# Performance work log

Measured on AMD Instinct MI355X. Metric: run time of the kernel, lower is better.

The kernel has to match this reference:

```python
import jax, jax.numpy as jnp
import numpy as np

N_SRC0, N_DST0 = 200000, 40000
N_SRC1, N_DST1 = 40000, 8000
E0, E1 = 1000000, 80000
D_IN, D_HID, D_OUT = 256, 512, 256


def setup_inputs() -> dict:
    key = jax.random.key(0)
    ks = jax.random.split(key, 10)
    return {
        "feat": jax.random.normal(ks[0], (N_SRC0, D_IN), dtype=jnp.float32),
        "Wself0": jax.random.normal(ks[1], (D_IN, D_HID), dtype=jnp.float32) * 0.05,
        "Wneigh0": jax.random.normal(ks[2], (D_IN, D_HID), dtype=jnp.float32) * 0.05,
        "b0": jnp.zeros((D_HID,), dtype=jnp.float32),
        "Wself1": jax.random.normal(ks[3], (D_HID, D_OUT), dtype=jnp.float32) * 0.05,
        "Wneigh1": jax.random.normal(ks[4], (D_HID, D_OUT), dtype=jnp.float32) * 0.05,
        "b1": jnp.zeros((D_OUT,), dtype=jnp.float32),
        "edge_src0": jax.random.randint(ks[5], (E0,), 0, N_SRC0, dtype=jnp.int32),
        "edge_dst0": jax.random.randint(ks[6], (E0,), 0, N_DST0, dtype=jnp.int32),
        "edge_src1": jax.random.randint(ks[7], (E1,), 0, N_SRC1, dtype=jnp.int32),
        "edge_dst1": jax.random.randint(ks[8], (E1,), 0, N_DST1, dtype=jnp.int32),
    }


def _mean_agg(h_src, src, dst, n_dst):
    # gather src features along edges, segment-mean over dst nodes
    msg_sum = jax.ops.segment_sum(h_src[src], dst, num_segments=n_dst)  # [n_dst, d]
    deg = jax.ops.segment_sum(jnp.ones(dst.shape, h_src.dtype), dst, num_segments=n_dst)
    return msg_sum / jnp.maximum(deg, 1.0)[:, None]


def _sage_layer(h, src, dst, n_dst, W_self, W_neigh, b):
    # DGL SAGEConv(mean): fc_self(h_dst) + fc_neigh(mean_neighbors) + bias
    h_dst = h[:n_dst]
    h_neigh = _mean_agg(h, src, dst, n_dst)
    return h_dst @ W_self + h_neigh @ W_neigh + b


def reference(feat, Wself0, Wneigh0, b0, Wself1, Wneigh1, b1,
              edge_src0, edge_dst0, edge_src1, edge_dst1):
    h = _sage_layer(feat, edge_src0, edge_dst0, N_DST0, Wself0, Wneigh0, b0)
    h = jax.nn.relu(h)  # ReLU between layers, not after last
    h = _sage_layer(h, edge_src1, edge_dst1, N_DST1, Wself1, Wneigh1, b1)
    return h
```

## Files before the change

### kernel.cpp

```cpp
#include <hip/hip_runtime.h>

#define DEV __device__ __forceinline__

typedef float f32x4 __attribute__((ext_vector_type(4)));
typedef short s16x4 __attribute__((ext_vector_type(4)));
typedef short s16x8 __attribute__((ext_vector_type(8)));

DEV float bf2f(short s) {
  unsigned u = ((unsigned)(unsigned short)s) << 16;
  return __builtin_bit_cast(float, u);
}
DEV short f2bf(float f) {
  unsigned u = __builtin_bit_cast(unsigned, f);
  u += 0x7FFFu + ((u >> 16) & 1u);
  return (short)(u >> 16);
}

DEV void gld_lds16(const void* g, void* l) {
  __builtin_amdgcn_global_load_lds(
      (const __attribute__((address_space(1))) void*)g,
      (__attribute__((address_space(3))) void*)l, 16, 0, 0);
}

__global__ void f32_to_bf16_k(const float* __restrict__ in, short* __restrict__ out, long n) {
  long i = ((long)blockIdx.x * blockDim.x + threadIdx.x) * 8;
  long stride = (long)gridDim.x * blockDim.x * 8;
  for (; i < n; i += stride) {
    f32x4 v0 = *(const f32x4*)(in + i);
    f32x4 v1 = *(const f32x4*)(in + i + 4);
    s16x8 o;
    o[0] = f2bf(v0[0]); o[1] = f2bf(v0[1]); o[2] = f2bf(v0[2]); o[3] = f2bf(v0[3]);
    o[4] = f2bf(v1[0]); o[5] = f2bf(v1[1]); o[6] = f2bf(v1[2]); o[7] = f2bf(v1[3]);
    *(s16x8*)(out + i) = o;
  }
}

__global__ void build_wt2_k(const float* __restrict__ Ws0, const float* __restrict__ Wn0,
                            short* __restrict__ W0T,
                            const float* __restrict__ Ws1, const float* __restrict__ Wn1,
                            short* __restrict__ W1T, int* __restrict__ cntz) {
  const int b = blockIdx.x, tid = threadIdx.x;
  if (b < 1024) {
    int idx = b * 256 + tid;
    if (idx < 512 * 512) {
      int n = idx >> 9, k = idx & 511;
      float v = (k < 256) ? Ws0[(size_t)k * 512 + n] : Wn0[(size_t)(k - 256) * 512 + n];
      W0T[idx] = f2bf(v);
    }
  } else if (b < 2048) {
    int idx = (b - 1024) * 256 + tid;
    if (idx < 256 * 1024) {
      int n = idx >> 10, k = idx & 1023;
      float v = (k < 512) ? Ws1[(size_t)k * 256 + n] : Wn1[(size_t)(k - 512) * 256 + n];
      W1T[idx] = f2bf(v);
    }
  } else {
    for (int idx = (b - 2048) * 256 + tid; idx < 48000; idx += 188 * 256) cntz[idx] = 0;
  }
}

__global__ void fillp2_k(const int* __restrict__ es0, const int* __restrict__ ed0, int E0,
                         int* __restrict__ cnt0, int* __restrict__ bk0,
                         const int* __restrict__ es1, const int* __restrict__ ed1, int E1,
                         int* __restrict__ cnt1, int* __restrict__ bk1) {
  const int b = blockIdx.x, tid = threadIdx.x;
  if (b < 936) {
    for (int e = b * 256 + tid; e < E0; e += 936 * 256) {
      int d = ed0[e];
      int p = atomicAdd(&cnt0[d], 1);
      if (p < 64) bk0[(d << 6) + p] = es0[e];
    }
  } else {
    for (int e = (b - 936) * 256 + tid; e < E1; e += 88 * 256) {
      int d = ed1[e];
      int p = atomicAdd(&cnt1[d], 1);
      if (p < 48) bk1[d * 48 + p] = es1[e];
    }
  }
}

__global__ void agg_f32_256(const float* __restrict__ X, const int* __restrict__ cntA,
                            const int* __restrict__ bucket, short* __restrict__ out,
                            int n_dst) {
  int gw = (blockIdx.x * blockDim.x + threadIdx.x) >> 6;
  if (gw >= n_dst) return;
  int lane = threadIdx.x & 63;
  int start = gw << 6, cnt = cntA[gw];
  float a[4] = {0, 0, 0, 0}, b[4] = {0, 0, 0, 0};
  int i = 0;
  for (; i + 2 <= cnt; i += 2) {
    int s0 = bucket[start + i], s1 = bucket[start + i + 1];
    f32x4 v0 = *(const f32x4*)(X + (size_t)s0 * 256 + lane * 4);
    f32x4 v1 = *(const f32x4*)(X + (size_t)s1 * 256 + lane * 4);
#pragma unroll
    for (int j = 0; j < 4; ++j) { a[j] += v0[j]; b[j] += v1[j]; }
  }
  if (i < cnt) {
    int s0 = bucket[start + i];
    f32x4 v0 = *(const f32x4*)(X + (size_t)s0 * 256 + lane * 4);
#pragma unroll
    for (int j = 0; j < 4; ++j) a[j] += v0[j];
  }
  float inv = 1.0f / (float)(cnt > 0 ? cnt : 1);
  s16x4 o;
#pragma unroll
  for (int j = 0; j < 4; ++j) o[j] = f2bf((a[j] + b[j]) * inv);
  *(s16x4*)(out + (size_t)gw * 256 + lane * 4) = o;
}

__global__ void agg_bf16_256(const short* __restrict__ X, const int* __restrict__ cntA,
                             const int* __restrict__ bucket, short* __restrict__ out,
                             int n_dst) {
  int gw = (blockIdx.x * blockDim.x + threadIdx.x) >> 6;
  if (gw >= n_dst) return;
  int lane = threadIdx.x & 63;
  int half = lane >> 5;
  int cl = lane & 31;
  int start = gw << 6, cnt = cntA[gw];
  float a[8] = {0, 0, 0, 0, 0, 0, 0, 0}, b[8] = {0, 0, 0, 0, 0, 0, 0, 0};
  int i = 0;
  for (; i + 8 <= cnt; i += 8) {
    int s0 = bucket[start + i + half];
    int s1 = bucket[start + i + 2 + half];
    int s2 = bucket[start + i + 4 + half];
    int s3 = bucket[start + i + 6 + half];
    s16x8 v0 = *(const s16x8*)(X + (size_t)s0 * 256 + cl * 8);
    s16x8 v1 = *(const s16x8*)(X + (size_t)s1 * 256 + cl * 8);
    s16x8 v2 = *(const s16x8*)(X + (size_t)s2 * 256 + cl * 8);
    s16x8 v3 = *(const s16x8*)(X + (size_t)s3 * 256 + cl * 8);
#pragma unroll
    for (int j = 0; j < 8; ++j) {
      a[j] += bf2f(v0[j]); b[j] += bf2f(v1[j]);
      a[j] += bf2f(v2[j]); b[j] += bf2f(v3[j]);
    }
  }
  for (; i + 4 <= cnt; i += 4) {
    int s0 = bucket[start + i + half];
    int s1 = bucket[start + i + 2 + half];
    s16x8 v0 = *(const s16x8*)(X + (size_t)s0 * 256 + cl * 8);
    s16x8 v1 = *(const s16x8*)(X + (size_t)s1 * 256 + cl * 8);
#pragma unroll
    for (int j = 0; j < 8; ++j) { a[j] += bf2f(v0[j]); b[j] += bf2f(v1[j]); }
  }
  for (; i < cnt; i += 2) {
    int idx = i + half;
    if (idx < cnt) {
      int s0 = bucket[start + idx];
      s16x8 v0 = *(const s16x8*)(X + (size_t)s0 * 256 + cl * 8);
#pragma unroll
      for (int j = 0; j < 8; ++j) a[j] += bf2f(v0[j]);
    }
  }
  float inv = 1.0f / (float)(cnt > 0 ? cnt : 1);
  float r[8];
#pragma unroll
  for (int j = 0; j < 8; ++j) {
    float s = a[j] + b[j];
    r[j] = s + __shfl(s, lane ^ 32);
  }
  if (half == 0) {
    s16x8 o;
#pragma unroll
    for (int j = 0; j < 8; ++j) o[j] = f2bf(r[j] * inv);
    *(s16x8*)(out + (size_t)gw * 256 + cl * 8) = o;
  }
}

__global__ void agg_bf16_512(const short* __restrict__ X, const int* __restrict__ cntA,
                             const int* __restrict__ bucket, short* __restrict__ out,
                             int n_dst) {
  int gw = (blockIdx.x * blockDim.x + threadIdx.x) >> 6;
  if (gw >= n_dst) return;
  int lane = threadIdx.x & 63;
  int start = gw * 48, cnt = cntA[gw];
  float a[8] = {0, 0, 0, 0, 0, 0, 0, 0}, b[8] = {0, 0, 0, 0, 0, 0, 0, 0};
  float c[8] = {0, 0, 0, 0, 0, 0, 0, 0}, d[8] = {0, 0, 0, 0, 0, 0, 0, 0};
  int i = 0;
  for (; i + 4 <= cnt; i += 4) {
    int s0 = bucket[start + i], s1 = bucket[start + i + 1];
    int s2 = bucket[start + i + 2], s3 = bucket[start + i + 3];
    s16x8 v0 = *(const s16x8*)(X + (size_t)s0 * 512 + lane * 8);
    s16x8 v1 = *(const s16x8*)(X + (size_t)s1 * 512 + lane * 8);
    s16x8 v2 = *(const s16x8*)(X + (size_t)s2 * 512 + lane * 8);
    s16x8 v3 = *(const s16x8*)(X + (size_t)s3 * 512 + lane * 8);
#pragma unroll
    for (int j = 0; j < 8; ++j) {
      a[j] += bf2f(v0[j]); b[j] += bf2f(v1[j]);
      c[j] += bf2f(v2[j]); d[j] += bf2f(v3[j]);
    }
  }
  for (; i < cnt; ++i) {
    int s0 = bucket[start + i];
    s16x8 v0 = *(const s16x8*)(X + (size_t)s0 * 512 + lane * 8);
#pragma unroll
    for (int j = 0; j < 8; ++j) a[j] += bf2f(v0[j]);
  }
  float inv = 1.0f / (float)(cnt > 0 ? cnt : 1);
  s16x8 o;
#pragma unroll
  for (int j = 0; j < 8; ++j) o[j] = f2bf(((a[j] + b[j]) + (c[j] + d[j])) * inv);
  *(s16x8*)(out + (size_t)gw * 512 + lane * 8) = o;
}

template <int BM, int BN, bool RELU_BF16>
__global__ __launch_bounds__(256, 2) void gemm_k(
    const short* __restrict__ Aleft, const short* __restrict__ Aright,
    const short* __restrict__ Bt, const float* __restrict__ bias,
    void* __restrict__ Cout, int M, int N, int K, int KH) {
  constexpr int MFR = BM / 32;
  constexpr int NFR = BN / 32;
  constexpr int PA = BM / 32;
  constexpr int PB = BN / 32;
  __shared__ short As[BM * 64];
  __shared__ short Bs[BN * 64];
  const int tid = threadIdx.x;
  const int w = tid >> 6, lane = tid & 63;
  const int m0 = blockIdx.y * BM, n0 = blockIdx.x * BN;
  const int wr = w >> 1, wc = w & 1;
  const int lr = lane & 15, lk = (lane >> 4) << 3;

  f32x4 acc[MFR][NFR] = {};

  const int nkt = K >> 6;
  const int ktH = KH >> 6;
  const size_t ldA = (size_t)KH * 2;
  const size_t ldB = (size_t)K * 2;

  for (int kt = 0; kt < nkt; ++kt) {
    const char* Abase = (const char*)((kt < ktH) ? Aleft : Aright);
    const int ktl = (kt < ktH) ? kt : kt - ktH;
#pragma unroll
    for (int j = 0; j < PA; ++j) {
      int c = w * PA + j;
      int o = (c << 10) + lane * 16;
      int row = o >> 7;
      int kb = o & 127;
      int kbs = kb ^ ((row & 7) << 4);
      int ar = m0 + row; if (ar > M - 1) ar = M - 1;
      gld_lds16(Abase + (size_t)ar * ldA + (size_t)(ktl * 128 + kbs),
                ((char*)As) + (c << 10));
    }
#pragma unroll
    for (int j = 0; j < PB; ++j) {
      int c = w * PB + j;
      int o = (c << 10) + lane * 16;
      int row = o >> 7;
      int kb = o & 127;
      int kbs = kb ^ ((row & 7) << 4);
      gld_lds16((const char*)Bt + (size_t)(n0 + row) * ldB + (size_t)(kt * 128 + kbs),
                ((char*)Bs) + (c << 10));
    }
    __syncthreads();
#pragma unroll
    for (int kk = 0; kk < 2; ++kk) {
      s16x8 af[MFR], bfr[NFR];
      const int kbyte = (kk * 32 + lk) * 2;
#pragma unroll
      for (int m = 0; m < MFR; ++m) {
        int r = wr * (BM / 2) + m * 16 + lr;
        af[m] = *(const s16x8*)((const char*)As + (r << 7) + (kbyte ^ ((r & 7) << 4)));
      }
#pragma unroll
      for (int n = 0; n < NFR; ++n) {
        int r = wc * (BN / 2) + n * 16 + lr;
        bfr[n] = *(const s16x8*)((const char*)Bs + (r << 7) + (kbyte ^ ((r & 7) << 4)));
      }
#pragma unroll
      for (int m = 0; m < MFR; ++m)
#pragma unroll
        for (int n = 0; n < NFR; ++n)
          acc[m][n] = __builtin_amdgcn_mfma_f32_16x16x32_bf16(af[m], bfr[n], acc[m][n], 0, 0, 0);
    }
    __syncthreads();
  }

  const int rq = (lane >> 4) * 4;
#pragma unroll
  for (int m = 0; m < MFR; ++m) {
#pragma unroll
    for (int n = 0; n < NFR; ++n) {
      const int col = n0 + wc * (BN / 2) + n * 16 + lr;
      const float bv = bias[col];
#pragma unroll
      for (int j = 0; j < 4; ++j) {
        const int row = m0 + wr * (BM / 2) + m * 16 + rq + j;
        if (row < M) {
          float v = acc[m][n][j] + bv;
          if (RELU_BF16) {
            v = v > 0.0f ? v : 0.0f;
            ((short*)Cout)[(size_t)row * N + col] = f2bf(v);
          } else {
            ((float*)Cout)[(size_t)row * N + col] = v;
          }
        }
      }
    }
  }
}

extern "C" void kernel_launch(void* const* d_in, const int* in_sizes, int n_in,
                              void* d_out, int out_size, void* d_ws, size_t ws_size,
                              hipStream_t stream) {
  const int NS0 = 200000, ND0 = 40000, ND1 = 8000;
  const int E0 = 1000000, E1 = 80000;
  const int DIN = 256, DH = 512, DOUT = 256;

  const float* feat = (const float*)d_in[0];
  const float* Wself0 = (const float*)d_in[1];
  const float* Wneigh0 = (const float*)d_in[2];
  const float* b0 = (const float*)d_in[3];
  const float* Wself1 = (const float*)d_in[4];
  const float* Wneigh1 = (const float*)d_in[5];
  const float* b1 = (const float*)d_in[6];
  const int* es0 = (const int*)d_in[7];
  const int* ed0 = (const int*)d_in[8];
  const int* es1 = (const int*)d_in[9];
  const int* ed1 = (const int*)d_in[10];

  char* w = (char*)d_ws;
  size_t pos = 0;
  auto take = [&](size_t b) -> char* {
    char* p = w + pos;
    pos += (b + 255) & ~(size_t)255;
    return p;
  };

  short* hne0 = (short*)take((size_t)ND0 * DIN * 2);
  short* h = (short*)take((size_t)ND0 * DH * 2);
  short* hne1 = (short*)take((size_t)ND1 * DH * 2);
  short* hdst0buf = (short*)take((size_t)ND0 * DIN * 2);
  short* W0T = (short*)take((size_t)DH * 2 * DIN * 2);
  short* W1T = (short*)take((size_t)DOUT * 2 * DH * 2);
  int* cnt0 = (int*)take((size_t)ND0 * 4);
  int* cnt1 = (int*)take((size_t)ND1 * 4);
  int* bucket0 = (int*)take((size_t)ND0 * 64 * 4);
  int* bucket1 = (int*)take((size_t)ND1 * 48 * 4);
  short* featbf = (short*)take((size_t)NS0 * DIN * 2);
  const bool use_bf = (ws_size >= pos);
  (void)in_sizes; (void)n_in; (void)out_size;

  const short* hdst0;
  if (use_bf) {
    f32_to_bf16_k<<<4096, 256, 0, stream>>>(feat, featbf, (long)NS0 * DIN);
    hdst0 = featbf;
  } else {
    f32_to_bf16_k<<<2048, 256, 0, stream>>>(feat, hdst0buf, (long)ND0 * DIN);
    hdst0 = hdst0buf;
  }

  build_wt2_k<<<2236, 256, 0, stream>>>(Wself0, Wneigh0, W0T, Wself1, Wneigh1, W1T, cnt0);

  fillp2_k<<<1024, 256, 0, stream>>>(es0, ed0, E0, cnt0, bucket0,
                                     es1, ed1, E1, cnt1, bucket1);

  if (use_bf)
    agg_bf16_256<<<ND0 / 4, 256, 0, stream>>>(featbf, cnt0, bucket0, hne0, ND0);
  else
    agg_f32_256<<<ND0 / 4, 256, 0, stream>>>(feat, cnt0, bucket0, hne0, ND0);

  gemm_k<128, 256, true><<<dim3(DH / 256, (ND0 + 127) / 128), 256, 0, stream>>>(
      hdst0, hne0, W0T, b0, h, ND0, DH, 2 * DIN, DIN);

  agg_bf16_512<<<ND1 / 4, 256, 0, stream>>>(h, cnt1, bucket1, hne1, ND1);

  gemm_k<64, 128, false><<<dim3(DOUT / 128, (ND1 + 63) / 64), 256, 0, stream>>>(
      h, hne1, W1T, b1, d_out, ND1, DOUT, 2 * DH, DH);
}
```

Measured before the change: 297.9 us.

## Fuse front-end prep kernels, memset counters, shrink layer-0 GEMM tile

Merges the feature bf16 conversion, weight transpose, and edge bucketing into a single front kernel, partitioned by block ranges. Counter zeroing moves to a hipMemsetAsync that runs first. The 8-wide unrolled gather loop in the 256-dim aggregation is dropped, and the layer-0 GEMM tile goes from 128x256 to 128x128 for more blocks. The aim is fewer launches and more overlap of independent prep work, but block ranges now share a fixed grid and the gather has less memory-level parallelism.

```diff
diff --git a/kernel.cpp b/kernel.cpp
--- a/kernel.cpp
+++ b/kernel.cpp
@@ -22,56 +22,48 @@
       (__attribute__((address_space(3))) void*)l, 16, 0, 0);
 }
 
-__global__ void f32_to_bf16_k(const float* __restrict__ in, short* __restrict__ out, long n) {
-  long i = ((long)blockIdx.x * blockDim.x + threadIdx.x) * 8;
-  long stride = (long)gridDim.x * blockDim.x * 8;
-  for (; i < n; i += stride) {
-    f32x4 v0 = *(const f32x4*)(in + i);
-    f32x4 v1 = *(const f32x4*)(in + i + 4);
-    s16x8 o;
-    o[0] = f2bf(v0[0]); o[1] = f2bf(v0[1]); o[2] = f2bf(v0[2]); o[3] = f2bf(v0[3]);
-    o[4] = f2bf(v1[0]); o[5] = f2bf(v1[1]); o[6] = f2bf(v1[2]); o[7] = f2bf(v1[3]);
-    *(s16x8*)(out + i) = o;
-  }
-}
-
-__global__ void build_wt2_k(const float* __restrict__ Ws0, const float* __restrict__ Wn0,
-                            short* __restrict__ W0T,
-                            const float* __restrict__ Ws1, const float* __restrict__ Wn1,
-                            short* __restrict__ W1T, int* __restrict__ cntz) {
+__global__ void front_k(const float* __restrict__ feat, short* __restrict__ fbf, long nconv,
+                        const float* __restrict__ Ws0, const float* __restrict__ Wn0,
+                        short* __restrict__ W0T,
+                        const float* __restrict__ Ws1, const float* __restrict__ Wn1,
+                        short* __restrict__ W1T,
+                        const int* __restrict__ es0, const int* __restrict__ ed0, int E0,
+                        int* __restrict__ cnt0, int* __restrict__ bk0,
+                        const int* __restrict__ es1, const int* __restrict__ ed1, int E1,
+                        int* __restrict__ cnt1, int* __restrict__ bk1) {
   const int b = blockIdx.x, tid = threadIdx.x;
-  if (b < 1024) {
-    int idx = b * 256 + tid;
-    if (idx < 512 * 512) {
-      int n = idx >> 9, k = idx & 511;
-      float v = (k < 256) ? Ws0[(size_t)k * 512 + n] : Wn0[(size_t)(k - 256) * 512 + n];
-      W0T[idx] = f2bf(v);
-    }
-  } else if (b < 2048) {
-    int idx = (b - 1024) * 256 + tid;
-    if (idx < 256 * 1024) {
-      int n = idx >> 10, k = idx & 1023;
-      float v = (k < 512) ? Ws1[(size_t)k * 256 + n] : Wn1[(size_t)(k - 512) * 256 + n];
-      W1T[idx] = f2bf(v);
-    }
-  } else {
-    for (int idx = (b - 2048) * 256 + tid; idx < 48000; idx += 188 * 256) cntz[idx] = 0;
-  }
-}
-
-__global__ void fillp2_k(const int* __restrict__ es0, const int* __restrict__ ed0, int E0,
-                         int* __restrict__ cnt0, int* __restrict__ bk0,
-                         const int* __restrict__ es1, const int* __restrict__ ed1, int E1,
-                         int* __restrict__ cnt1, int* __restrict__ bk1) {
-  const int b = blockIdx.x, tid = threadIdx.x;
-  if (b < 936) {
-    for (int e = b * 256 + tid; e < E0; e += 936 * 256) {
+  if (b < 1664) {
+    long i = ((long)b * 256 + tid) * 8;
+    const long stride = (long)1664 * 256 * 8;
+    for (; i < nconv; i += stride) {
+      f32x4 v0 = *(const f32x4*)(feat + i);
+      f32x4 v1 = *(const f32x4*)(feat + i + 4);
+      s16x8 o;
+      o[0] = f2bf(v0[0]); o[1] = f2bf(v0[1]); o[2] = f2bf(v0[2]); o[3] = f2bf(v0[3]);
+      o[4] = f2bf(v1[0]); o[5] = f2bf(v1[1]); o[6] = f2bf(v1[2]); o[7] = f2bf(v1[3]);
+      *(s16x8*)(fbf + i) = o;
+    }
+  } else if (b < 1728) {
+    for (int idx = (b - 1664) * 256 + tid; idx < 524288; idx += 64 * 256) {
+      if (idx < 262144) {
+        int n = idx >> 9, k = idx & 511;
+        float v = (k < 256) ? Ws0[(size_t)k * 512 + n] : Wn0[(size_t)(k - 256) * 512 + n];
+        W0T[idx] = f2bf(v);
+      } else {
+        int i2 = idx - 262144;
+        int n = i2 >> 10, k = i2 & 1023;
+        float v = (k < 512) ? Ws1[(size_t)k * 256 + n] : Wn1[(size_t)(k - 512) * 256 + n];
+        W1T[i2] = f2bf(v);
+      }
+    }
+  } else if (b < 2016) {
+    for (int e = (b - 1728) * 256 + tid; e < E0; e += 288 * 256) {
       int d = ed0[e];
       int p = atomicAdd(&cnt0[d], 1);
       if (p < 64) bk0[(d << 6) + p] = es0[e];
     }
   } else {
-    for (int e = (b - 936) * 256 + tid; e < E1; e += 88 * 256) {
+    for (int e = (b - 2016) * 256 + tid; e < E1; e += 32 * 256) {
       int d = ed1[e];
       int p = atomicAdd(&cnt1[d], 1);
       if (p < 48) bk1[d * 48 + p] = es1[e];
@@ -119,21 +111,6 @@
   int start = gw << 6, cnt = cntA[gw];
   float a[8] = {0, 0, 0, 0, 0, 0, 0, 0}, b[8] = {0, 0, 0, 0, 0, 0, 0, 0};
   int i = 0;
-  for (; i + 8 <= cnt; i += 8) {
-    int s0 = bucket[start + i + half];
-    int s1 = bucket[start + i + 2 + half];
-    int s2 = bucket[start + i + 4 + half];
-    int s3 = bucket[start + i + 6 + half];
-    s16x8 v0 = *(const s16x8*)(X + (size_t)s0 * 256 + cl * 8);
-    s16x8 v1 = *(const s16x8*)(X + (size_t)s1 * 256 + cl * 8);
-    s16x8 v2 = *(const s16x8*)(X + (size_t)s2 * 256 + cl * 8);
-    s16x8 v3 = *(const s16x8*)(X + (size_t)s3 * 256 + cl * 8);
-#pragma unroll
-    for (int j = 0; j < 8; ++j) {
-      a[j] += bf2f(v0[j]); b[j] += bf2f(v1[j]);
-      a[j] += bf2f(v2[j]); b[j] += bf2f(v3[j]);
-    }
-  }
   for (; i + 4 <= cnt; i += 4) {
     int s0 = bucket[start + i + half];
     int s1 = bucket[start + i + 2 + half];
@@ -339,26 +316,23 @@
   const bool use_bf = (ws_size >= pos);
   (void)in_sizes; (void)n_in; (void)out_size;
 
-  const short* hdst0;
-  if (use_bf) {
-    f32_to_bf16_k<<<4096, 256, 0, stream>>>(feat, featbf, (long)NS0 * DIN);
-    hdst0 = featbf;
-  } else {
-    f32_to_bf16_k<<<2048, 256, 0, stream>>>(feat, hdst0buf, (long)ND0 * DIN);
-    hdst0 = hdst0buf;
-  }
-
-  build_wt2_k<<<2236, 256, 0, stream>>>(Wself0, Wneigh0, W0T, Wself1, Wneigh1, W1T, cnt0);
-
-  fillp2_k<<<1024, 256, 0, stream>>>(es0, ed0, E0, cnt0, bucket0,
-                                     es1, ed1, E1, cnt1, bucket1);
+  hipMemsetAsync(cnt0, 0, (size_t)(ND0 + ND1) * 4, stream);
+
+  const short* hdst0 = use_bf ? featbf : hdst0buf;
+
+  front_k<<<2048, 256, 0, stream>>>(
+      feat, use_bf ? featbf : hdst0buf,
+      use_bf ? (long)NS0 * DIN : (long)ND0 * DIN,
+      Wself0, Wneigh0, W0T, Wself1, Wneigh1, W1T,
+      es0, ed0, E0, cnt0, bucket0,
+      es1, ed1, E1, cnt1, bucket1);
 
   if (use_bf)
     agg_bf16_256<<<ND0 / 4, 256, 0, stream>>>(featbf, cnt0, bucket0, hne0, ND0);
   else
     agg_f32_256<<<ND0 / 4, 256, 0, stream>>>(feat, cnt0, bucket0, hne0, ND0);
 
-  gemm_k<128, 256, true><<<dim3(DH / 256, (ND0 + 127) / 128), 256, 0, stream>>>(
+  gemm_k<128, 128, true><<<dim3(DH / 128, (ND0 + 127) / 128), 256, 0, stream>>>(
       hdst0, hne0, W0T, b0, h, ND0, DH, 2 * DIN, DIN);
 
   agg_bf16_512<<<ND1 / 4, 256, 0, stream>>>(h, cnt1, bucket1, hne1, ND1);
```

New measurement: 250.4 us, median of 2. 16.0% less time.
